# Performance work log

Measured on AMD Instinct MI355X. Metric: run time of the kernel, lower is better.

The kernel has to match this reference:

```python
import jax, jax.numpy as jnp
import numpy as np

N_NODES = 100000
D = 128


def setup_inputs() -> dict:
    key = jax.random.key(0)
    ks = jax.random.split(key, 6)
    x = jax.random.normal(ks[0], (N_NODES, 300), dtype=jnp.float32)
    n_id = jnp.arange(N_NODES, dtype=jnp.int64)
    edge_index = jax.random.randint(ks[1], (2, 1600000), 0, N_NODES, dtype=jnp.int64)
    history = jax.random.randint(ks[2], (4096, 50), 0, N_NODES, dtype=jnp.int64)
    candidates = jax.random.randint(ks[3], (4096, 20), 0, N_NODES, dtype=jnp.int64)
    W_enc = jax.random.normal(ks[4], (300, D), dtype=jnp.float32) * 0.05
    W_gnn = jax.random.normal(ks[5], (D, D), dtype=jnp.float32) * 0.05
    return {"x": x, "n_id": n_id, "edge_index": edge_index,
            "history": history, "candidates": candidates,
            "W_enc": W_enc, "W_gnn": W_gnn}


def reference(x, n_id, edge_index, history, candidates, W_enc, W_gnn):
    N = x.shape[0]
    # news encoder: linear projection of raw node features -> [N, D]
    news_emb = x @ W_enc
    # gnn: mean aggregation over incoming edges, then linear
    src, dst = edge_index[0], edge_index[1]
    agg = jax.ops.segment_sum(news_emb[src], dst, num_segments=N)      # [N, D]
    deg = jax.ops.segment_sum(jnp.ones((src.shape[0], 1), news_emb.dtype), dst,
                              num_segments=N)                          # [N, 1]
    struct_emb = (agg / jnp.maximum(deg, 1.0)) @ W_gnn
    xx = news_emb + struct_emb                                          # [N, D]
    # scatter into dense lookup table (n_id == arange -> max_id == N, static)
    news_lookup = jnp.zeros((N, xx.shape[1]), xx.dtype).at[n_id].set(xx)
    # gather histories / candidates
    history_embs = news_lookup[history]                                 # [B, H, D]
    cand_embs = news_lookup[candidates]                                 # [B, C, D]
    mask = (history != 0).astype(xx.dtype)                              # [B, H]
    sum_embs = jnp.einsum('bhd,bh->bd', history_embs, mask)
    num_read = jnp.clip(mask.sum(axis=1, keepdims=True), 1e-9, None)
    user_vec = sum_embs / num_read                                      # [B, D]
    scores = jnp.einsum('bcd,bd->bc', cand_embs, user_vec)              # [B, C]
    return scores
```

## Files before the change

### kernel.cpp

```cpp
#include <hip/hip_runtime.h>

#define NN 100000
#define DD 128
#define KE 300
#define NE 1600000
#define NB 4096
#define HL 50
#define CL 20

#define NBUCK 1563
#define SLOT  1280
#define PBLK  250
#define EPB   6400
#define EPT   25
#define EBLK  1563
#define ENCB  256

#define WTE_N 40960
#define WTG_N 16384
#define PREPB ((WTE_N + WTG_N + 255) / 256)

typedef unsigned short ushort_t;
typedef unsigned char uchar_t;
using bf16x8 = __attribute__((ext_vector_type(8))) short;
using f32x4  = __attribute__((ext_vector_type(4))) float;
using v2f    = __attribute__((ext_vector_type(2))) float;

union U4B { uint4 u; bf16x8 b; unsigned a[4]; };

__device__ __forceinline__ ushort_t f2bf(float f) {
    unsigned u = __float_as_uint(f);
    unsigned r = u + 0x7FFF + ((u >> 16) & 1);
    return (ushort_t)(r >> 16);
}
__device__ __forceinline__ float bf2f(unsigned s) {
    return __uint_as_float(s << 16);
}
__device__ __forceinline__ bf16x8 pack8(float4 a, float4 b) {
    U4B r;
    r.a[0] = (unsigned)f2bf(a.x) | ((unsigned)f2bf(a.y) << 16);
    r.a[1] = (unsigned)f2bf(a.z) | ((unsigned)f2bf(a.w) << 16);
    r.a[2] = (unsigned)f2bf(b.x) | ((unsigned)f2bf(b.y) << 16);
    r.a[3] = (unsigned)f2bf(b.z) | ((unsigned)f2bf(b.w) << 16);
    return r.b;
}

__device__ __forceinline__ bf16x8 loadA8m(const float* __restrict__ x,
                                          int row, int col, bool rowok) {
    float v[8];
#pragma unroll
    for (int j = 0; j < 8; ++j) {
        int c = col + j;
        v[j] = (rowok && c < KE) ? x[(long long)row * KE + c] : 0.f;
    }
    return pack8(make_float4(v[0], v[1], v[2], v[3]),
                 make_float4(v[4], v[5], v[6], v[7]));
}

__global__ __launch_bounds__(256) void k_wprep(const float* __restrict__ We,
                                               const float* __restrict__ Wg,
                                               ushort_t* __restrict__ wte,
                                               ushort_t* __restrict__ wtg) {
    int i = blockIdx.x * 256 + threadIdx.x;
    if (i < WTE_N) {
        int j = i & 7, lane = (i >> 3) & 63, cf = (i >> 9) & 7, ch = i >> 12;
        int k = ch * 32 + (lane >> 4) * 8 + j;
        int n = cf * 16 + (lane & 15);
        wte[i] = f2bf((k < KE) ? We[k * DD + n] : 0.f);
    } else if (i < WTE_N + WTG_N) {
        int t = i - WTE_N;
        int j = t & 7, lane = (t >> 3) & 63, cf = (t >> 9) & 7, ks = t >> 12;
        int k = ks * 32 + (lane >> 4) * 8 + j;
        int n = cf * 16 + (lane & 15);
        wtg[t] = f2bf(Wg[k * DD + n]);
    }
}

__global__ __launch_bounds__(256, 1) void k_encpart(const float* __restrict__ x,
                                                    const ushort_t* __restrict__ wtF,
                                                    const int* __restrict__ ei,
                                                    unsigned* __restrict__ gcur,
                                                    unsigned* __restrict__ pairs,
                                                    ushort_t* __restrict__ news,
                                                    uchar_t* __restrict__ nf8) {
    __shared__ __align__(16) char smem[3 * NBUCK * 4];
    const int tid = threadIdx.x;

    if (blockIdx.x < PBLK) {
        unsigned* sh = (unsigned*)smem;
        unsigned* sb = sh + NBUCK;
        unsigned* sc = sb + NBUCK;
        const int eb = blockIdx.x * EPB;
        for (int i = tid; i < NBUCK; i += 256) sh[i] = 0;
        __syncthreads();

        unsigned val[EPT], bk[EPT];
#pragma unroll
        for (int l = 0; l < EPT; ++l) {
            int e = eb + l * 256 + tid;
            unsigned src = (unsigned)ei[e];
            unsigned dst = (unsigned)ei[NE + e];
            val[l] = (src << 6) | (dst & 63u);
            bk[l] = dst >> 6;
            atomicAdd(&sh[bk[l]], 1u);
        }
        __syncthreads();

        for (int i = tid; i < NBUCK; i += 256) {
            unsigned h = sh[i];
            sb[i] = (unsigned)i * SLOT + (h ? atomicAdd(&gcur[i], h) : 0u);
            sc[i] = 0;
        }
        __syncthreads();

#pragma unroll
        for (int l = 0; l < EPT; ++l) {
            unsigned b = bk[l];
            unsigned pos = sb[b] + atomicAdd(&sc[b], 1u);
            if (pos < (b + 1u) * SLOT) pairs[pos] = val[l];
        }
        return;
    }

    uchar_t* f8s = (uchar_t*)smem;
    const int w = tid >> 6, lane = tid & 63;
    const int hl = lane & 15, kg = lane >> 4;

    bf16x8 B[10][8];
#pragma unroll
    for (int c = 0; c < 10; ++c)
#pragma unroll
        for (int cf = 0; cf < 8; ++cf)
            B[c][cf] = *(const bf16x8*)&wtF[(c * 8 + cf) * 512 + lane * 8];

    for (int tile = blockIdx.x - PBLK; tile < EBLK; tile += ENCB) {
        const int row0 = tile * 64 + w * 16;
        const int r0 = row0 + hl;
        const bool ok0 = r0 < NN;
        const float* xr = &x[(long long)r0 * KE + kg * 8];
        const float4 fz = make_float4(0.f, 0.f, 0.f, 0.f);

        float4 ra[9][2];
        if (ok0) {
#pragma unroll
            for (int c = 0; c < 9; ++c) {
                const float4* p = (const float4*)(xr + c * 32);
                ra[c][0] = p[0];
                ra[c][1] = p[1];
            }
        } else {
#pragma unroll
            for (int c = 0; c < 9; ++c) { ra[c][0] = fz; ra[c][1] = fz; }
        }
        bf16x8 a9 = loadA8m(x, r0, 288 + kg * 8, ok0);

        f32x4 acc[8];
#pragma unroll
        for (int j = 0; j < 8; ++j) acc[j] = (f32x4)0.f;

#pragma unroll
        for (int c = 0; c < 9; ++c) {
            bf16x8 a = pack8(ra[c][0], ra[c][1]);
#pragma unroll
            for (int cf = 0; cf < 8; ++cf)
                acc[cf] = __builtin_amdgcn_mfma_f32_16x16x32_bf16(a, B[c][cf], acc[cf], 0, 0, 0);
        }
#pragma unroll
        for (int cf = 0; cf < 8; ++cf)
            acc[cf] = __builtin_amdgcn_mfma_f32_16x16x32_bf16(a9, B[9][cf], acc[cf], 0, 0, 0);

#pragma unroll
        for (int cf = 0; cf < 8; ++cf)
#pragma unroll
            for (int j = 0; j < 4; ++j) {
                int lr = w * 16 + kg * 4 + j;
                int grow = tile * 64 + lr;
                int gcol = cf * 16 + hl;
                if (grow < NN)
                    news[(long long)grow * DD + gcol] = f2bf(acc[cf][j]);
                int p = __builtin_amdgcn_cvt_pk_fp8_f32(acc[cf][j], 0.f, 0, false);
                f8s[lr * DD + gcol] = (uchar_t)(p & 0xFF);
            }
        __syncthreads();
        {
            int r = tid >> 2, boff = (tid & 3) * 32;
            int grow = tile * 64 + r;
            if (grow < NN) {
                const uint4* s = (const uint4*)&f8s[r * DD + boff];
                uint4* d = (uint4*)&nf8[(long long)grow * DD + boff];
                d[0] = s[0];
                d[1] = s[1];
            }
        }
        __syncthreads();
    }
}

__global__ __launch_bounds__(512) void k_baggnn(const unsigned* __restrict__ gcur,
                                                const unsigned* __restrict__ pairs,
                                                const uchar_t* __restrict__ nf8,
                                                const ushort_t* __restrict__ news,
                                                const ushort_t* __restrict__ wtF,
                                                ushort_t* __restrict__ xxb) {
    __shared__ unsigned srcs[SLOT];
    __shared__ unsigned hist[64], base[64], cur[64];
    __shared__ ushort_t aggs[64 * DD];
    const int tid = threadIdx.x;
    const int b = blockIdx.x;
    int cnt = (int)gcur[b];
    if (cnt > SLOT) cnt = SLOT;

    if (tid < 64) hist[tid] = 0;
    __syncthreads();
    for (int i = tid; i < cnt; i += 512)
        atomicAdd(&hist[pairs[b * SLOT + i] & 63u], 1u);
    __syncthreads();

    if (tid < 64) {
        unsigned h = hist[tid], v = h;
#pragma unroll
        for (int off = 1; off < 64; off <<= 1) {
            unsigned n = __shfl_up(v, off);
            if (tid >= off) v += n;
        }
        base[tid] = v - h;
        cur[tid]  = v - h;
    }
    __syncthreads();

    for (int i = tid; i < cnt; i += 512) {
        unsigned v = pairs[b * SLOT + i];
        srcs[atomicAdd(&cur[v & 63u], 1u)] = v >> 6;
    }
    __syncthreads();

    const int w = tid >> 6, lane = tid & 63;
    const int e = lane >> 4, l = lane & 15;
    for (int d = w; d < 64; d += 8) {
        int gd = b * 64 + d;
        if (gd >= NN) break;
        int s0 = (int)base[d], c = (int)hist[d];
        float acc[8];
#pragma unroll
        for (int j = 0; j < 8; ++j) acc[j] = 0.f;

        uint2 v = make_uint2(0u, 0u);
        if (e < c)
            v = *(const uint2*)&nf8[(long long)srcs[s0 + e] * DD + l * 8];
        for (int i = 4; i < c; i += 4) {
            uint2 vn = make_uint2(0u, 0u);
            int ii = i + e;
            if (ii < c)
                vn = *(const uint2*)&nf8[(long long)srcs[s0 + ii] * DD + l * 8];
            v2f d0 = __builtin_amdgcn_cvt_pk_f32_fp8((int)v.x, false);
            v2f d1 = __builtin_amdgcn_cvt_pk_f32_fp8((int)v.x, true);
            acc[0] += d0[0]; acc[1] += d0[1]; acc[2] += d1[0]; acc[3] += d1[1];
            d0 = __builtin_amdgcn_cvt_pk_f32_fp8((int)v.y, false);
            d1 = __builtin_amdgcn_cvt_pk_f32_fp8((int)v.y, true);
            acc[4] += d0[0]; acc[5] += d0[1]; acc[6] += d1[0]; acc[7] += d1[1];
            v = vn;
        }
        {
            v2f d0 = __builtin_amdgcn_cvt_pk_f32_fp8((int)v.x, false);
            v2f d1 = __builtin_amdgcn_cvt_pk_f32_fp8((int)v.x, true);
            acc[0] += d0[0]; acc[1] += d0[1]; acc[2] += d1[0]; acc[3] += d1[1];
            d0 = __builtin_amdgcn_cvt_pk_f32_fp8((int)v.y, false);
            d1 = __builtin_amdgcn_cvt_pk_f32_fp8((int)v.y, true);
            acc[4] += d0[0]; acc[5] += d0[1]; acc[6] += d1[0]; acc[7] += d1[1];
        }

#pragma unroll
        for (int j = 0; j < 8; ++j) {
            acc[j] += __shfl_xor(acc[j], 16);
            acc[j] += __shfl_xor(acc[j], 32);
        }
        if (e == 0) {
            uint4 o;
            o.x = (unsigned)f2bf(acc[0]) | ((unsigned)f2bf(acc[1]) << 16);
            o.y = (unsigned)f2bf(acc[2]) | ((unsigned)f2bf(acc[3]) << 16);
            o.z = (unsigned)f2bf(acc[4]) | ((unsigned)f2bf(acc[5]) << 16);
            o.w = (unsigned)f2bf(acc[6]) | ((unsigned)f2bf(acc[7]) << 16);
            *(uint4*)&aggs[d * DD + (l ^ (d & 15)) * 8] = o;
        }
    }
    __syncthreads();

    const int hl = lane & 15, kg = lane >> 4;
    const int rw = (w & 3) * 16;
    const int cfb = (w >> 2) * 4;
    U4B a[4];
#pragma unroll
    for (int ks = 0; ks < 4; ++ks)
        a[ks].u = *(const uint4*)&aggs[(rw + hl) * DD + ((ks * 4 + kg) ^ hl) * 8];

    f32x4 acc[4];
#pragma unroll
    for (int j = 0; j < 4; ++j) acc[j] = (f32x4)0.f;

#pragma unroll
    for (int ks = 0; ks < 4; ++ks) {
        const ushort_t* bp = &wtF[(ks * 8 + cfb) * 512 + lane * 8];
#pragma unroll
        for (int cf = 0; cf < 4; ++cf) {
            bf16x8 bfr = *(const bf16x8*)&bp[cf * 512];
            acc[cf] = __builtin_amdgcn_mfma_f32_16x16x32_bf16(a[ks].b, bfr, acc[cf], 0, 0, 0);
        }
    }

#pragma unroll
    for (int j = 0; j < 4; ++j) {
        int lr = rw + kg * 4 + j;
        int grow = b * 64 + lr;
        if (grow < NN) {
            float s = 1.f / fmaxf((float)hist[lr], 1.f);
#pragma unroll
            for (int cf = 0; cf < 4; ++cf) {
                int gcol = (cfb + cf) * 16 + hl;
                float nv = bf2f((unsigned)news[(long long)grow * DD + gcol]);
                xxb[(long long)grow * DD + gcol] = f2bf(nv + acc[cf][j] * s);
            }
        }
    }
}

__global__ __launch_bounds__(128) void k_user(const int* __restrict__ hist,
                                              const int* __restrict__ cand,
                                              const ushort_t* __restrict__ xxb,
                                              float* __restrict__ out) {
    __shared__ float part[2][128];
    __shared__ float cnts[2];
    __shared__ float uvs[128];
    const int b = blockIdx.x, t = threadIdx.x;
    const int w = t >> 6, lane = t & 63;

    float s0 = 0.f, s1 = 0.f, cnt = 0.f;
    for (int h = w; h < HL; h += 2) {
        int id = hist[b * HL + h];
        if (id != 0) {
            unsigned v = *(const unsigned*)&xxb[(long long)id * DD + lane * 2];
            s0 += bf2f(v & 0xFFFFu);
            s1 += bf2f(v >> 16);
            cnt += 1.f;
        }
    }
    part[w][lane * 2]     = s0;
    part[w][lane * 2 + 1] = s1;
    if (lane == 0) cnts[w] = cnt;
    __syncthreads();

    float inv = 1.f / fmaxf(cnts[0] + cnts[1], 1e-9f);
    uvs[t] = (part[0][t] + part[1][t]) * inv;
    __syncthreads();

    float2 uvp = *(const float2*)&uvs[lane * 2];
    for (int c = w; c < CL; c += 2) {
        int id = cand[b * CL + c];
        unsigned v = *(const unsigned*)&xxb[(long long)id * DD + lane * 2];
        float p = uvp.x * bf2f(v & 0xFFFFu) + uvp.y * bf2f(v >> 16);
#pragma unroll
        for (int off = 32; off >= 1; off >>= 1) p += __shfl_xor(p, off);
        if (lane == 0) out[b * CL + c] = p;
    }
}

extern "C" void kernel_launch(void* const* d_in, const int* in_sizes, int n_in,
                              void* d_out, int out_size, void* d_ws, size_t ws_size,
                              hipStream_t stream) {
    const float* x    = (const float*)d_in[0];
    const int*   ei   = (const int*)d_in[2];
    const int*   hist = (const int*)d_in[3];
    const int*   cand = (const int*)d_in[4];
    const float* Wenc = (const float*)d_in[5];
    const float* Wgnn = (const float*)d_in[6];
    float* out = (float*)d_out;

    ushort_t* news_bf = (ushort_t*)d_ws;
    ushort_t* xx_bf   = news_bf + (size_t)NN * DD;
    ushort_t* wt_enc  = xx_bf + (size_t)NN * DD;
    ushort_t* wt_gnn  = wt_enc + WTE_N;
    uchar_t*  news_f8 = (uchar_t*)(wt_gnn + WTG_N);
    unsigned* gcur    = (unsigned*)(news_f8 + (size_t)NN * DD);
    unsigned* pairs   = gcur + NBUCK;

    hipMemsetAsync(gcur, 0, NBUCK * sizeof(unsigned), stream);

    k_wprep<<<PREPB, 256, 0, stream>>>(Wenc, Wgnn, wt_enc, wt_gnn);
    k_encpart<<<PBLK + ENCB, 256, 0, stream>>>(x, wt_enc, ei, gcur, pairs,
                                               news_bf, news_f8);
    k_baggnn<<<NBUCK, 512, 0, stream>>>(gcur, pairs, news_f8, news_bf, wt_gnn, xx_bf);
    k_user<<<NB, 128, 0, stream>>>(hist, cand, xx_bf, out);
}
```

Baseline: 145.6 us.

## Pipeline encoder x loads into per-wave LDS ring with async global_load_lds

Replaces the register-staged per-tile load of x in the encoder with a per-wave 4-slot LDS ring buffer. Each slot is filled by `global_load_lds` three K-chunks ahead, and explicit `s_waitcnt vmcnt` waits let loads overlap the MFMA work. The block-wide `__syncthreads` around the fp8 staging is replaced by per-wave staging, so each wave runs independently. In exchange it uses much more LDS, and the last K-chunk now reads past column 300 into the next row instead of zero-masking. That relies on the zero-padded weights, which only gives correct results if those extra values are finite.

```diff
diff --git a/kernel.cpp b/kernel.cpp
--- a/kernel.cpp
+++ b/kernel.cpp
@@ -20,6 +20,8 @@
 #define WTG_N 16384
 #define PREPB ((WTE_N + WTG_N + 255) / 256)
 
+#define CBYTES 2304
+
 typedef unsigned short ushort_t;
 typedef unsigned char uchar_t;
 using bf16x8 = __attribute__((ext_vector_type(8))) short;
@@ -43,18 +45,6 @@
     r.a[2] = (unsigned)f2bf(b.x) | ((unsigned)f2bf(b.y) << 16);
     r.a[3] = (unsigned)f2bf(b.z) | ((unsigned)f2bf(b.w) << 16);
     return r.b;
-}
-
-__device__ __forceinline__ bf16x8 loadA8m(const float* __restrict__ x,
-                                          int row, int col, bool rowok) {
-    float v[8];
-#pragma unroll
-    for (int j = 0; j < 8; ++j) {
-        int c = col + j;
-        v[j] = (rowok && c < KE) ? x[(long long)row * KE + c] : 0.f;
-    }
-    return pack8(make_float4(v[0], v[1], v[2], v[3]),
-                 make_float4(v[4], v[5], v[6], v[7]));
 }
 
 __global__ __launch_bounds__(256) void k_wprep(const float* __restrict__ We,
@@ -83,7 +73,7 @@
                                                     unsigned* __restrict__ pairs,
                                                     ushort_t* __restrict__ news,
                                                     uchar_t* __restrict__ nf8) {
-    __shared__ __align__(16) char smem[3 * NBUCK * 4];
+    __shared__ __align__(16) char smem[45056];
     const int tid = threadIdx.x;
 
     if (blockIdx.x < PBLK) {
@@ -122,9 +112,10 @@
         return;
     }
 
-    uchar_t* f8s = (uchar_t*)smem;
     const int w = tid >> 6, lane = tid & 63;
     const int hl = lane & 15, kg = lane >> 4;
+    char* cbw = smem + w * (4 * CBYTES);
+    uchar_t* fsw = (uchar_t*)(smem + 36864 + w * 2048);
 
     bf16x8 B[10][8];
 #pragma unroll
@@ -133,67 +124,88 @@
         for (int cf = 0; cf < 8; ++cf)
             B[c][cf] = *(const bf16x8*)&wtF[(c * 8 + cf) * 512 + lane * 8];
 
-    for (int tile = blockIdx.x - PBLK; tile < EBLK; tile += ENCB) {
-        const int row0 = tile * 64 + w * 16;
-        const int r0 = row0 + hl;
-        const bool ok0 = r0 < NN;
-        const float* xr = &x[(long long)r0 * KE + kg * 8];
-        const float4 fz = make_float4(0.f, 0.f, 0.f, 0.f);
-
-        float4 ra[9][2];
-        if (ok0) {
-#pragma unroll
-            for (int c = 0; c < 9; ++c) {
-                const float4* p = (const float4*)(xr + c * 32);
-                ra[c][0] = p[0];
-                ra[c][1] = p[1];
+    const int t0 = blockIdx.x - PBLK;
+    const int NT = 1 + (EBLK - 1 - t0) / ENCB;
+    const int last = NT * 10 - 1;
+    const long long NNKE = (long long)NN * KE;
+
+#define ISSUE(n)                                                                \
+    do {                                                                        \
+        int kk_ = (n) / 10, cc_ = (n) - kk_ * 10;                               \
+        int tile_ = t0 + kk_ * ENCB;                                            \
+        int brow_ = tile_ * 64 + w * 16;                                        \
+        char* dstb_ = cbw + ((n) & 3) * CBYTES;                                 \
+        _Pragma("unroll")                                                       \
+        for (int q = 0; q < 3; ++q) {                                           \
+            int g = q * 64 + lane;                                              \
+            int r = g / 9, j = g - r * 9;                                       \
+            if (g < 144 && j != 8) {                                            \
+                long long idx = (long long)(brow_ + r) * KE + cc_ * 32 + j * 4; \
+                if (brow_ + r >= NN || idx > NNKE - 4) idx = 0;                 \
+                __builtin_amdgcn_global_load_lds(                               \
+                    (const __attribute__((address_space(1))) unsigned*)&x[idx], \
+                    (__attribute__((address_space(3))) unsigned*)(dstb_ + q * 1024), \
+                    16, 0, 0);                                                  \
+            }                                                                   \
+        }                                                                       \
+    } while (0)
+
+    f32x4 acc[8];
+#pragma unroll
+    for (int j = 0; j < 8; ++j) acc[j] = (f32x4)0.f;
+
+    ISSUE(0);
+    ISSUE(1);
+    ISSUE(2);
+
+    for (int i = 0; i <= last; ++i) {
+        if (i + 3 <= last) ISSUE(i + 3);
+        int ahead = last - i;
+        if (ahead >= 3)      asm volatile("s_waitcnt vmcnt(9)" ::: "memory");
+        else if (ahead == 2) asm volatile("s_waitcnt vmcnt(6)" ::: "memory");
+        else if (ahead == 1) asm volatile("s_waitcnt vmcnt(3)" ::: "memory");
+        else                 asm volatile("s_waitcnt vmcnt(0)" ::: "memory");
+
+        const int kk = i / 10, c = i - kk * 10;
+        const ushort_t* cb = (const ushort_t*)(cbw + (i & 3) * CBYTES);
+        float4 v0 = *(const float4*)(cb + (hl * 9 + kg * 2) * 8);
+        float4 v1 = *(const float4*)(cb + (hl * 9 + kg * 2 + 1) * 8);
+        bf16x8 a = pack8(v0, v1);
+#pragma unroll
+        for (int cf = 0; cf < 8; ++cf)
+            acc[cf] = __builtin_amdgcn_mfma_f32_16x16x32_bf16(a, B[c][cf], acc[cf], 0, 0, 0);
+
+        if (c == 9) {
+            const int tile = t0 + kk * ENCB;
+            const int row0 = tile * 64 + w * 16;
+#pragma unroll
+            for (int cf = 0; cf < 8; ++cf)
+#pragma unroll
+                for (int j = 0; j < 4; ++j) {
+                    int lr = kg * 4 + j;
+                    int grow = row0 + lr;
+                    int gcol = cf * 16 + hl;
+                    if (grow < NN)
+                        news[(long long)grow * DD + gcol] = f2bf(acc[cf][j]);
+                    int p = __builtin_amdgcn_cvt_pk_fp8_f32(acc[cf][j], 0.f, 0, false);
+                    fsw[lr * DD + gcol] = (uchar_t)(p & 0xFF);
+                }
+            asm volatile("" ::: "memory");
+            {
+                int lr = lane >> 2;
+                int grow = row0 + lr;
+                if (grow < NN) {
+                    const uint4* s = (const uint4*)(fsw + lane * 32);
+                    uint4* d = (uint4*)&nf8[(long long)grow * DD + (lane & 3) * 32];
+                    d[0] = s[0];
+                    d[1] = s[1];
+                }
             }
-        } else {
-#pragma unroll
-            for (int c = 0; c < 9; ++c) { ra[c][0] = fz; ra[c][1] = fz; }
-        }
-        bf16x8 a9 = loadA8m(x, r0, 288 + kg * 8, ok0);
-
-        f32x4 acc[8];
-#pragma unroll
-        for (int j = 0; j < 8; ++j) acc[j] = (f32x4)0.f;
-
-#pragma unroll
-        for (int c = 0; c < 9; ++c) {
-            bf16x8 a = pack8(ra[c][0], ra[c][1]);
-#pragma unroll
-            for (int cf = 0; cf < 8; ++cf)
-                acc[cf] = __builtin_amdgcn_mfma_f32_16x16x32_bf16(a, B[c][cf], acc[cf], 0, 0, 0);
-        }
-#pragma unroll
-        for (int cf = 0; cf < 8; ++cf)
-            acc[cf] = __builtin_amdgcn_mfma_f32_16x16x32_bf16(a9, B[9][cf], acc[cf], 0, 0, 0);
-
-#pragma unroll
-        for (int cf = 0; cf < 8; ++cf)
-#pragma unroll
-            for (int j = 0; j < 4; ++j) {
-                int lr = w * 16 + kg * 4 + j;
-                int grow = tile * 64 + lr;
-                int gcol = cf * 16 + hl;
-                if (grow < NN)
-                    news[(long long)grow * DD + gcol] = f2bf(acc[cf][j]);
-                int p = __builtin_amdgcn_cvt_pk_fp8_f32(acc[cf][j], 0.f, 0, false);
-                f8s[lr * DD + gcol] = (uchar_t)(p & 0xFF);
-            }
-        __syncthreads();
-        {
-            int r = tid >> 2, boff = (tid & 3) * 32;
-            int grow = tile * 64 + r;
-            if (grow < NN) {
-                const uint4* s = (const uint4*)&f8s[r * DD + boff];
-                uint4* d = (uint4*)&nf8[(long long)grow * DD + boff];
-                d[0] = s[0];
-                d[1] = s[1];
-            }
-        }
-        __syncthreads();
-    }
+#pragma unroll
+            for (int j = 0; j < 8; ++j) acc[j] = (f32x4)0.f;
+        }
+    }
+#undef ISSUE
 }
 
 __global__ __launch_bounds__(512) void k_baggnn(const unsigned* __restrict__ gcur,
```

Measured after the change: 243.2 us. 67.0% more time.
